# Kernel optimization log

Hardware: AMD Instinct MI355X
Metric: run time of the kernel (lower is better)

## Reference

```python
import jax, jax.numpy as jnp
import numpy as np

N_JOINT = 32
N_EDGE = N_JOINT * (N_JOINT - 1)  # 992, fully-connected directed, no self loops
IN_ENC = 150   # 3 * source_seq_len
NH, NO = 256, 128   # node hidden / node out (node_hidden_dim = edge_hidden_dim in source)
EH, EO = 256, 128   # edge hidden / edge out
DEC_IN = 3
T, B = 25, 16
NUM_PASSING = 2


def _incidence():
    send, rec = np.nonzero(~np.eye(N_JOINT, dtype=bool))
    R = np.zeros((N_EDGE, N_JOINT), np.float32)
    S = np.zeros((N_EDGE, N_JOINT), np.float32)
    R[np.arange(N_EDGE), rec] = 1.0
    S[np.arange(N_EDGE), send] = 1.0
    return jnp.asarray(R), jnp.asarray(S)


def _mlp(x, w1, b1, w2, b2):
    # Linear -> ReLU -> (Dropout p=0) -> Linear -> ReLU
    return jax.nn.relu(jax.nn.relu(x @ w1 + b1) @ w2 + b2)


def _node2edge(x, R, S):
    # x: [B, N, D] -> [B, E, 2D] (sends then recs, as in source)
    sends = jnp.einsum('en,bnd->bed', S, x)
    recs = jnp.einsum('en,bnd->bed', R, x)
    return jnp.concatenate([sends, recs], axis=-1)


def _edge2node(x, R):
    # x: [B, E, D] -> [B, N, D], mean over incoming edges
    inc = jnp.einsum('en,bed->bnd', R, x)
    return inc / R.sum(0)[:, None]


def setup_inputs() -> dict:
    key = jax.random.key(0)
    ks = jax.random.split(key, 24)
    R, S = _incidence()

    def lin(k, i, o):
        return jax.random.normal(k, (i, o), jnp.float32) * (2.0 / (i + o)) ** 0.5

    b = lambda o: jnp.full((o,), 0.1, jnp.float32)
    inp = {
        'encoder_input': jax.random.normal(ks[0], (B, N_JOINT, IN_ENC), jnp.float32),
        'decoder_input': jax.random.normal(ks[1], (T, B, N_JOINT, DEC_IN), jnp.float32),
        'rec_encode': R, 'send_encode': S,
        # encoder mlp1: IN_ENC -> NH -> NO
        'enc_w1': lin(ks[2], IN_ENC, NH), 'enc_b1': b(NH),
        'enc_w2': lin(ks[3], NH, NO), 'enc_b2': b(NO),
        # passing edge MLP: 2*NO -> EH -> EO
        'pe_w1': lin(ks[4], 2 * NO, EH), 'pe_b1': b(EH),
        'pe_w2': lin(ks[5], EH, EO), 'pe_b2': b(EO),
        # passing node MLP: EO -> NH -> NO
        'pn_w1': lin(ks[6], EO, NH), 'pn_b1': b(NH),
        'pn_w2': lin(ks[7], NH, NO), 'pn_b2': b(NO),
        # decoder node2edge MLP: 2*NO -> EH -> EO
        'de_w1': lin(ks[8], 2 * NO, EH), 'de_b1': b(EH),
        'de_w2': lin(ks[9], EH, EO), 'de_b2': b(EO),
        # GRU-like gates; input_size = DEC_IN + EO
        'w_hr': lin(ks[10], NO, NO), 'w_hi': lin(ks[11], NO, NO), 'w_hn': lin(ks[12], NO, NO),
        'w_ir': lin(ks[13], EO + DEC_IN, NO), 'b_ir': b(NO),
        'w_ii': lin(ks[14], EO + DEC_IN, NO), 'b_ii': b(NO),
        'w_in': lin(ks[15], EO + DEC_IN, NO), 'b_in': b(NO),
    }
    return inp


def reference(encoder_input, decoder_input, rec_encode, send_encode,
              enc_w1, enc_b1, enc_w2, enc_b2,
              pe_w1, pe_b1, pe_w2, pe_b2,
              pn_w1, pn_b1, pn_w2, pn_b2,
              de_w1, de_b1, de_w2, de_b2,
              w_hr, w_hi, w_hn, w_ir, b_ir, w_ii, b_ii, w_in, b_in):
    R, S = rec_encode, send_encode
    # ---- encoder ----
    x = _mlp(encoder_input, enc_w1, enc_b1, enc_w2, enc_b2)  # [B,N,NO]
    for _ in range(NUM_PASSING):
        x = _mlp(_node2edge(x, R, S), pe_w1, pe_b1, pe_w2, pe_b2)  # [B,E,EO]
        x = _mlp(_edge2node(x, R), pn_w1, pn_b1, pn_w2, pn_b2)     # [B,N,NO]
    node_hidden = x

    # ---- decoder: GRU-style recurrent message passing ----
    def step(h, inp):
        e = _mlp(_node2edge(h, R, S), de_w1, de_b1, de_w2, de_b2)  # [B,E,EO]
        msg = _edge2node(e, R)                                      # [B,N,EO]
        ni = jnp.concatenate([msg, inp], axis=-1)                   # [B,N,EO+3]
        r = jax.nn.sigmoid(ni @ w_ir + b_ir + h @ w_hr)
        i = jax.nn.sigmoid(ni @ w_ii + b_ii + h @ w_hi)
        n = jnp.tanh(ni @ w_in + b_in + r * (h @ w_hn))
        h_new = (1.0 - i) * n + i * h
        return h_new, h_new

    state, outputs = jax.lax.scan(step, node_hidden, decoder_input)
    return outputs, state
```

## Files before the change

kernel.cpp:

```cpp
#include <hip/hip_runtime.h>


#define TSTEPS 25

typedef _Float16 half_t;
typedef __attribute__((ext_vector_type(8))) _Float16 half8;
typedef __attribute__((ext_vector_type(8))) short short8;
typedef __attribute__((ext_vector_type(4))) float f32x4;

#define OFF_ENC_W1T 0
#define OFF_ENC_W2T 40960
#define OFF_PE_W1T  73728
#define OFF_PE_W2T  139264
#define OFF_PN_W1T  172032
#define OFF_PN_W2T  204800
#define OFF_DE_W1T  237568
#define OFF_DE_W2T  303104
#define OFF_WGT     335872
#define WTOTAL      483328

__device__ __align__(16) half_t g_wf16[WTOTAL];
__device__ __align__(16) float g_hbuf[2 * 512 * 128];
__device__ __align__(16) float g_msg[512 * 128];

__device__ __forceinline__ half8 h8zero() {
    half8 z;
    #pragma unroll
    for (int e = 0; e < 8; ++e) z[e] = (half_t)0.f;
    return z;
}
__device__ __forceinline__ half8 relu8(half8 x) {
    short8 s = *(short8*)&x;
    short8 m = s >> 15;
    s = s & ~m;
    return *(half8*)&s;
}
#define MFMA(a, b, c) __builtin_amdgcn_mfma_f32_16x16x32_f16((a), (b), (c), 0, 0, 0)
#define BFRAG(off, tile, KS, kk) ((off) + (((tile) * (KS) + (kk)) << 9) + m16 * 32 + quad * 8)

__global__ void convert_kernel(const float* __restrict__ enc_w1, const float* __restrict__ enc_w2,
                               const float* __restrict__ pe_w1, const float* __restrict__ pe_w2,
                               const float* __restrict__ pn_w1, const float* __restrict__ pn_w2,
                               const float* __restrict__ de_w1, const float* __restrict__ de_w2,
                               const float* __restrict__ w_hr, const float* __restrict__ w_hi,
                               const float* __restrict__ w_hn, const float* __restrict__ w_ir,
                               const float* __restrict__ w_ii, const float* __restrict__ w_in) {
    const int idx = blockIdx.x * 256 + threadIdx.x;
    if (idx >= WTOTAL) return;
    float v = 0.f;
    if (idx < OFF_ENC_W2T) {
        int s = idx, e = s & 7, quad = (s >> 3) & 3, m16 = (s >> 5) & 15, t = s >> 9;
        int kk = t % 5, nt = t / 5;
        int j = nt * 16 + m16, k = kk * 32 + quad * 8 + e;
        v = (k < 150) ? enc_w1[k * 256 + j] : 0.f;
    } else if (idx < OFF_PE_W1T) {
        int s = idx - OFF_ENC_W2T, e = s & 7, quad = (s >> 3) & 3, m16 = (s >> 5) & 15, t = s >> 9;
        int kk = t & 7, nt = t >> 3;
        int j = nt * 16 + m16, k = kk * 32 + quad * 8 + e;
        v = enc_w2[k * 128 + j];
    } else if (idx < OFF_PE_W2T) {
        int s = idx - OFF_PE_W1T, e = s & 7, quad = (s >> 3) & 3, m16 = (s >> 5) & 15, t = s >> 9;
        int kk = t & 3, nt = t >> 2;
        int j = nt * 16 + m16, k = kk * 32 + quad * 8 + e;
        v = pe_w1[(k + ((j >= 256) ? 128 : 0)) * 256 + (j & 255)];
    } else if (idx < OFF_PN_W1T) {
        int s = idx - OFF_PE_W2T, e = s & 7, quad = (s >> 3) & 3, m16 = (s >> 5) & 15, t = s >> 9;
        int kk = t & 7, nt = t >> 3;
        int j = nt * 16 + m16, k = kk * 32 + quad * 8 + e;
        v = pe_w2[k * 128 + j];
    } else if (idx < OFF_PN_W2T) {
        int s = idx - OFF_PN_W1T, e = s & 7, quad = (s >> 3) & 3, m16 = (s >> 5) & 15, t = s >> 9;
        int kk = t & 3, nt = t >> 2;
        int j = nt * 16 + m16, k = kk * 32 + quad * 8 + e;
        v = pn_w1[k * 256 + j];
    } else if (idx < OFF_DE_W1T) {
        int s = idx - OFF_PN_W2T, e = s & 7, quad = (s >> 3) & 3, m16 = (s >> 5) & 15, t = s >> 9;
        int kk = t & 7, nt = t >> 3;
        int j = nt * 16 + m16, k = kk * 32 + quad * 8 + e;
        v = pn_w2[k * 128 + j];
    } else if (idx < OFF_DE_W2T) {
        int s = idx - OFF_DE_W1T, e = s & 7, quad = (s >> 3) & 3, m16 = (s >> 5) & 15, t = s >> 9;
        int kk = t & 3, nt = t >> 2;
        int j = nt * 16 + m16, k = kk * 32 + quad * 8 + e;
        v = de_w1[(k + ((j >= 256) ? 128 : 0)) * 256 + (j & 255)];
    } else if (idx < OFF_WGT) {
        int s = idx - OFF_DE_W1T - (OFF_DE_W2T - OFF_DE_W1T), e = s & 7, quad = (s >> 3) & 3, m16 = (s >> 5) & 15, t = s >> 9;
        int kk = t & 7, nt = t >> 3;
        int j = nt * 16 + m16, k = kk * 32 + quad * 8 + e;
        v = de_w2[k * 128 + j];
    } else {
        int s = idx - OFF_WGT, e = s & 7, quad = (s >> 3) & 3, m16 = (s >> 5) & 15, t = s >> 9;
        int kk = t % 9, ct = t / 9;
        int c = ct * 16 + m16, k = kk * 32 + quad * 8 + e;
        int grp = (c >> 5) & 3, j = ((c >> 7) << 5) | (c & 31);
        if (grp == 0)
            v = (k < 128) ? w_ir[k * 128 + j] : (k < 256) ? w_hr[(k - 128) * 128 + j]
              : (k < 259) ? w_ir[(128 + k - 256) * 128 + j] : 0.f;
        else if (grp == 1)
            v = (k < 128) ? w_ii[k * 128 + j] : (k < 256) ? w_hi[(k - 128) * 128 + j]
              : (k < 259) ? w_ii[(128 + k - 256) * 128 + j] : 0.f;
        else if (grp == 2)
            v = (k < 128) ? w_in[k * 128 + j]
              : (k >= 256 && k < 259) ? w_in[(128 + k - 256) * 128 + j] : 0.f;
        else
            v = (k >= 128 && k < 256) ? w_hn[(k - 128) * 128 + j] : 0.f;
    }
    g_wf16[idx] = (half_t)v;
}

__global__ void __launch_bounds__(512, 2)
encoder_kernel(const float* __restrict__ enc_in,
               const float* __restrict__ enc_b1, const float* __restrict__ enc_b2) {
    const int b = blockIdx.x & 15;
    const int sub = blockIdx.x >> 4;
    const int tid = threadIdx.x;
    const int wave = tid >> 6;
    const int lane = tid & 63;
    const int m16 = lane & 15, quad = lane >> 4;
    const int r0 = sub * 4;

    __shared__ __align__(16) half_t s_enc[32 * 168];
    __shared__ __align__(16) half_t s_hid[32 * 264];

    for (int i = tid; i < 32 * 168; i += 512) {
        const int s = i / 168, k = i - s * 168;
        s_enc[i] = (half_t)((k < 150) ? enc_in[((size_t)b * 32 + s) * 150 + k] : 0.f);
    }
    __syncthreads();
    #pragma unroll
    for (int i = 0; i < 4; ++i) {
        const int ti = wave + i * 8;
        const int nt = ti & 15, mt = ti >> 4;
        f32x4 acc = (f32x4)(0.f);
        #pragma unroll
        for (int k = 0; k < 5; ++k) {
            half8 a  = *(const half8*)&s_enc[(mt * 16 + m16) * 168 + k * 32 + quad * 8];
            half8 bf = *(const half8*)&g_wf16[BFRAG(OFF_ENC_W1T, nt, 5, k)];
            acc = MFMA(a, bf, acc);
        }
        const int j = nt * 16 + m16;
        const float bj = enc_b1[j];
        #pragma unroll
        for (int g = 0; g < 4; ++g)
            s_hid[(mt * 16 + quad * 4 + g) * 264 + j] = (half_t)fmaxf(acc[g] + bj, 0.f);
    }
    __syncthreads();
    float* h0 = g_hbuf + (size_t)b * 32 * 128;
    #pragma unroll
    for (int i = 0; i < 2; ++i) {
        const int ti = wave + i * 8;
        const int nt = ti & 7, mt = ti >> 3;
        f32x4 acc = (f32x4)(0.f);
        #pragma unroll
        for (int k = 0; k < 8; ++k) {
            half8 a  = *(const half8*)&s_hid[(mt * 16 + m16) * 264 + k * 32 + quad * 8];
            half8 bf = *(const half8*)&g_wf16[BFRAG(OFF_ENC_W2T, nt, 8, k)];
            acc = MFMA(a, bf, acc);
        }
        if (mt == (sub >> 2) && quad == (sub & 3)) {
            const int j = nt * 16 + m16;
            const float bj = enc_b2[j];
            #pragma unroll
            for (int g = 0; g < 4; ++g)
                h0[(r0 + g) * 128 + j] = fmaxf(acc[g] + bj, 0.f);
        }
    }
}

template <int IS_DEC>
__global__ void __launch_bounds__(512, 1)
edge_kernel(int parity, const float* __restrict__ b1, const float* __restrict__ b2) {
    const int b = blockIdx.x >> 4;
    const int rq = blockIdx.x & 15;
    const int r0 = rq * 2;
    const int tid = threadIdx.x;
    const int wave = tid >> 6;
    const int lane = tid & 63;
    const int m16 = lane & 15, quad = lane >> 4;

    __shared__ __align__(16) half_t s_hh[32 * 136];
    __shared__ __align__(16) half_t s_P[32 * 264];
    __shared__ __align__(16) half_t s_Qb[2 * 264];

    {
        const float* hsrc = g_hbuf + (size_t)parity * 512 * 128 + (size_t)b * 32 * 128;
        const int i = tid * 8;
        const int row = i >> 7, col = i & 127;
        const float* sp = hsrc + row * 128 + col;
        half8 h0;
        #pragma unroll
        for (int e = 0; e < 8; ++e) h0[e] = (half_t)sp[e];
        *(half8*)&s_hh[row * 136 + col] = h0;
    }
    __syncthreads();

    {
        const int woff = IS_DEC ? OFF_DE_W1T : OFF_PE_W1T;
        const int rmt = r0 >> 4, rloc0 = r0 & 15;
        #pragma unroll
        for (int i = 0; i < 6; ++i) {
            const int ti = wave + 8 * i;
            const bool isQ = ti >= 32;
            const int nt = isQ ? (ti - 32) : (ti & 15);
            const int mt = isQ ? rmt : (ti >> 4);
            const int brow = isQ ? (nt + 16) : nt;
            f32x4 acc = (f32x4)(0.f);
            #pragma unroll
            for (int k = 0; k < 4; ++k) {
                half8 a = *(const half8*)&s_hh[(mt * 16 + m16) * 136 + k * 32 + quad * 8];
                half8 bf = *(const half8*)&g_wf16[BFRAG(woff, brow, 4, k)];
                acc = MFMA(a, bf, acc);
            }
            const int j = nt * 16 + m16;
            if (!isQ) {
                #pragma unroll
                for (int g = 0; g < 4; ++g)
                    s_P[(mt * 16 + quad * 4 + g) * 264 + j] = (half_t)acc[g];
            } else {
                const float bj = b1[j];
                #pragma unroll
                for (int g = 0; g < 4; ++g) {
                    const int rr = quad * 4 + g;
                    if (rr == rloc0)     s_Qb[j] = (half_t)(acc[g] + bj);
                    if (rr == rloc0 + 1) s_Qb[264 + j] = (half_t)(acc[g] + bj);
                }
            }
        }
    }
    __syncthreads();

    {
        const int woff2 = IS_DEC ? OFF_DE_W2T : OFF_PE_W2T;
        const int nt = wave;
        half8 qb[2][8];
        #pragma unroll
        for (int ri = 0; ri < 2; ++ri)
            #pragma unroll
            for (int k = 0; k < 8; ++k)
                qb[ri][k] = *(const half8*)&s_Qb[ri * 264 + k * 32 + quad * 8];
        f32x4 acc[2][2];
        #pragma unroll
        for (int ri = 0; ri < 2; ++ri)
            #pragma unroll
            for (int mt = 0; mt < 2; ++mt) acc[ri][mt] = (f32x4)(0.f);
        #pragma unroll
        for (int k = 0; k < 8; ++k) {
            half8 bf = *(const half8*)&g_wf16[BFRAG(woff2, nt, 8, k)];
            #pragma unroll
            for (int mt = 0; mt < 2; ++mt) {
                half8 pv = *(const half8*)&s_P[(mt * 16 + m16) * 264 + k * 32 + quad * 8];
                #pragma unroll
                for (int ri = 0; ri < 2; ++ri) {
                    half8 hv = relu8(pv + qb[ri][k]);
                    if (mt * 16 + m16 == r0 + ri) hv = h8zero();
                    acc[ri][mt] = MFMA(hv, bf, acc[ri][mt]);
                }
            }
        }
        const float b2n = b2[nt * 16 + m16];
        #pragma unroll
        for (int ri = 0; ri < 2; ++ri) {
            float pp = 0.f;
            #pragma unroll
            for (int mt = 0; mt < 2; ++mt)
                #pragma unroll
                for (int g = 0; g < 4; ++g)
                    pp += fmaxf(acc[ri][mt][g] + b2n, 0.f);
            pp += __shfl_xor(pp, 16);
            pp += __shfl_xor(pp, 32);
            if (quad == 0)
                g_msg[((size_t)b * 32 + r0 + ri) * 128 + nt * 16 + m16] =
                    (pp - fmaxf(b2n, 0.f)) * (1.f / 31.f);
        }
    }
}

__global__ void __launch_bounds__(256, 4)
node_kernel(int parity_out, const float* __restrict__ pn_b1, const float* __restrict__ pn_b2) {
    const int mt16 = blockIdx.x;
    const int tid = threadIdx.x;
    const int wave = tid >> 6;
    const int lane = tid & 63;
    const int m16 = lane & 15, quad = lane >> 4;

    __shared__ __align__(16) half_t s_A[16 * 136];
    __shared__ __align__(16) half_t s_H[16 * 264];

    {
        const int i = tid * 8;
        const int row = i >> 7, col = i & 127;
        const float* sp = g_msg + ((size_t)mt16 * 16 + row) * 128 + col;
        half8 h0;
        #pragma unroll
        for (int e = 0; e < 8; ++e) h0[e] = (half_t)sp[e];
        *(half8*)&s_A[row * 136 + col] = h0;
    }
    __syncthreads();
    #pragma unroll
    for (int i = 0; i < 4; ++i) {
        const int nt = wave + 4 * i;
        f32x4 acc = (f32x4)(0.f);
        #pragma unroll
        for (int k = 0; k < 4; ++k) {
            half8 a = *(const half8*)&s_A[m16 * 136 + k * 32 + quad * 8];
            half8 bf = *(const half8*)&g_wf16[BFRAG(OFF_PN_W1T, nt, 4, k)];
            acc = MFMA(a, bf, acc);
        }
        const int j = nt * 16 + m16;
        const float bj = pn_b1[j];
        #pragma unroll
        for (int g = 0; g < 4; ++g)
            s_H[(quad * 4 + g) * 264 + j] = (half_t)fmaxf(acc[g] + bj, 0.f);
    }
    __syncthreads();
    float* h_next = g_hbuf + (size_t)parity_out * 512 * 128;
    #pragma unroll
    for (int i = 0; i < 2; ++i) {
        const int nt = wave + 4 * i;
        f32x4 acc = (f32x4)(0.f);
        #pragma unroll
        for (int k = 0; k < 8; ++k) {
            half8 a = *(const half8*)&s_H[m16 * 264 + k * 32 + quad * 8];
            half8 bf = *(const half8*)&g_wf16[BFRAG(OFF_PN_W2T, nt, 8, k)];
            acc = MFMA(a, bf, acc);
        }
        const int j = nt * 16 + m16;
        const float bj = pn_b2[j];
        #pragma unroll
        for (int g = 0; g < 4; ++g)
            h_next[((size_t)mt16 * 16 + quad * 4 + g) * 128 + j] = fmaxf(acc[g] + bj, 0.f);
    }
}

__global__ void __launch_bounds__(256, 4)
gru_kernel(int parity, int t,
           const float* __restrict__ b_ir, const float* __restrict__ b_ii,
           const float* __restrict__ b_in,
           const float* __restrict__ dec_in, float* __restrict__ out) {
    const int b = blockIdx.x >> 3;
    const int nt = (blockIdx.x >> 1) & 3;
    const int mt2 = blockIdx.x & 1;
    const int rbase = mt2 * 16;
    const int tid = threadIdx.x;
    const int wave = tid >> 6;
    const int lane = tid & 63;
    const int m16 = lane & 15, quad = lane >> 4;
    const float* hsrc = g_hbuf + (size_t)parity * 512 * 128 + (size_t)b * 32 * 128;

    __shared__ __align__(16) half_t s_A[16 * 296];
    __shared__ __align__(16) half_t s_g[16 * 136];

    {
        const int i = tid * 8;
        const int row = i >> 7, col = i & 127;
        const float* mp = g_msg + ((size_t)b * 32 + rbase + row) * 128 + col;
        const float* hp = hsrc + (rbase + row) * 128 + col;
        half8 m0, h0;
        #pragma unroll
        for (int e = 0; e < 8; ++e) { m0[e] = (half_t)mp[e]; h0[e] = (half_t)hp[e]; }
        *(half8*)&s_A[row * 296 + col] = m0;
        *(half8*)&s_A[row * 296 + 128 + col] = h0;
    }
    for (int i = tid; i < 16 * 32; i += 256) {
        const int row = i >> 5, c = i & 31;
        s_A[row * 296 + 256 + c] = (c < 3)
            ? (half_t)dec_in[(((size_t)t * 16 + b) * 32 + rbase + row) * 3 + c] : (half_t)0.f;
    }
    __syncthreads();

    #pragma unroll
    for (int i = 0; i < 2; ++i) {
        const int nt2 = wave + 4 * i;
        const int ct = nt * 8 + nt2;
        f32x4 acc = (f32x4)(0.f);
        #pragma unroll
        for (int k = 0; k < 9; ++k) {
            half8 a = *(const half8*)&s_A[m16 * 296 + k * 32 + quad * 8];
            half8 bf = *(const half8*)&g_wf16[BFRAG(OFF_WGT, ct, 9, k)];
            acc = MFMA(a, bf, acc);
        }
        #pragma unroll
        for (int g = 0; g < 4; ++g)
            s_g[(quad * 4 + g) * 136 + nt2 * 16 + m16] = (half_t)acc[g];
    }
    __syncthreads();

    float* h_next = g_hbuf + (size_t)(parity ^ 1) * 512 * 128 + (size_t)b * 32 * 128;
    #pragma unroll
    for (int e = 0; e < 2; ++e) {
        const int idx = tid + 256 * e;
        const int row = idx >> 5, jl = idx & 31;
        const int j = nt * 32 + jl;
        const float rs = (float)s_g[row * 136 + jl] + b_ir[j];
        const float is = (float)s_g[row * 136 + 32 + jl] + b_ii[j];
        const float ns = (float)s_g[row * 136 + 64 + jl] + b_in[j];
        const float hn = (float)s_g[row * 136 + 96 + jl];
        const float rr = 1.f / (1.f + __expf(-rs));
        const float ii = 1.f / (1.f + __expf(-is));
        const float nn = tanhf(ns + rr * hn);
        const float hold = hsrc[(rbase + row) * 128 + j];
        const float hnew = (1.f - ii) * nn + ii * hold;
        h_next[(rbase + row) * 128 + j] = hnew;
        const size_t grow = (size_t)b * 32 + rbase + row;
        out[(size_t)t * 512 * 128 + grow * 128 + j] = hnew;
        if (t == TSTEPS - 1)
            out[(size_t)TSTEPS * 512 * 128 + grow * 128 + j] = hnew;
    }
}

extern "C" void kernel_launch(void* const* d_in, const int* in_sizes, int n_in,
                              void* d_out, int out_size, void* d_ws, size_t ws_size,
                              hipStream_t stream) {
    const float* enc_in = (const float*)d_in[0];
    const float* dec_in = (const float*)d_in[1];
    const float* enc_w1 = (const float*)d_in[4];
    const float* enc_b1 = (const float*)d_in[5];
    const float* enc_w2 = (const float*)d_in[6];
    const float* enc_b2 = (const float*)d_in[7];
    const float* pe_w1 = (const float*)d_in[8];
    const float* pe_b1 = (const float*)d_in[9];
    const float* pe_w2 = (const float*)d_in[10];
    const float* pe_b2 = (const float*)d_in[11];
    const float* pn_w1 = (const float*)d_in[12];
    const float* pn_b1 = (const float*)d_in[13];
    const float* pn_w2 = (const float*)d_in[14];
    const float* pn_b2 = (const float*)d_in[15];
    const float* de_w1 = (const float*)d_in[16];
    const float* de_b1 = (const float*)d_in[17];
    const float* de_w2 = (const float*)d_in[18];
    const float* de_b2 = (const float*)d_in[19];
    const float* w_hr = (const float*)d_in[20];
    const float* w_hi = (const float*)d_in[21];
    const float* w_hn = (const float*)d_in[22];
    const float* w_ir = (const float*)d_in[23];
    const float* b_ir = (const float*)d_in[24];
    const float* w_ii = (const float*)d_in[25];
    const float* b_ii = (const float*)d_in[26];
    const float* w_in = (const float*)d_in[27];
    const float* b_in = (const float*)d_in[28];
    (void)d_ws; (void)ws_size; (void)in_sizes; (void)n_in;

    convert_kernel<<<(WTOTAL + 255) / 256, 256, 0, stream>>>(
        enc_w1, enc_w2, pe_w1, pe_w2, pn_w1, pn_w2, de_w1, de_w2,
        w_hr, w_hi, w_hn, w_ir, w_ii, w_in);

    encoder_kernel<<<128, 512, 0, stream>>>(enc_in, enc_b1, enc_b2);

    int p = 0;
    for (int pass = 0; pass < 2; ++pass) {
        edge_kernel<0><<<256, 512, 0, stream>>>(p, pe_b1, pe_b2);
        node_kernel<<<32, 256, 0, stream>>>(p ^ 1, pn_b1, pn_b2);
        p ^= 1;
    }
    float* out = (float*)d_out;
    for (int t = 0; t < TSTEPS; ++t) {
        edge_kernel<1><<<256, 512, 0, stream>>>(p, de_b1, de_b2);
        gru_kernel<<<128, 256, 0, stream>>>(p, t, b_ir, b_ii, b_in, dec_in, out);
        p ^= 1;
    }
}
```

Baseline: 445.4 us.

## Fuse node MLP and GRU update into edge kernel, dropping global message buffer

Folds the node MLP (encoder passes) and the GRU gate computation (decoder steps) into the edge kernel's epilogue. Each block keeps its two-row message in shared memory and runs the follow-up MFMAs on padded 16-row tiles where only 2 rows are valid. This halves the number of kernel launches per step and removes the g_msg round trip through global memory. In exchange, much of the follow-up MFMA work is spent on zero rows, and every block re-reads the gate and node weights.

```diff
diff --git a/kernel.cpp b/kernel.cpp
--- a/kernel.cpp
+++ b/kernel.cpp
@@ -21,7 +21,6 @@
 
 __device__ __align__(16) half_t g_wf16[WTOTAL];
 __device__ __align__(16) float g_hbuf[2 * 512 * 128];
-__device__ __align__(16) float g_msg[512 * 128];
 
 __device__ __forceinline__ half8 h8zero() {
     half8 z;
@@ -34,6 +33,14 @@
     short8 m = s >> 15;
     s = s & ~m;
     return *(half8*)&s;
+}
+__device__ __forceinline__ half8 frag_from_f32(const float* base) {
+    f32x4 a = *(const f32x4*)base;
+    f32x4 c = *(const f32x4*)(base + 4);
+    half8 h;
+    #pragma unroll
+    for (int e = 0; e < 4; ++e) { h[e] = (half_t)a[e]; h[4 + e] = (half_t)c[e]; }
+    return h;
 }
 #define MFMA(a, b, c) __builtin_amdgcn_mfma_f32_16x16x32_f16((a), (b), (c), 0, 0, 0)
 #define BFRAG(off, tile, KS, kk) ((off) + (((tile) * (KS) + (kk)) << 9) + m16 * 32 + quad * 8)
@@ -84,7 +91,7 @@
         int j = nt * 16 + m16, k = kk * 32 + quad * 8 + e;
         v = de_w1[(k + ((j >= 256) ? 128 : 0)) * 256 + (j & 255)];
     } else if (idx < OFF_WGT) {
-        int s = idx - OFF_DE_W1T - (OFF_DE_W2T - OFF_DE_W1T), e = s & 7, quad = (s >> 3) & 3, m16 = (s >> 5) & 15, t = s >> 9;
+        int s = idx - OFF_DE_W2T, e = s & 7, quad = (s >> 3) & 3, m16 = (s >> 5) & 15, t = s >> 9;
         int kk = t & 7, nt = t >> 3;
         int j = nt * 16 + m16, k = kk * 32 + quad * 8 + e;
         v = de_w2[k * 128 + j];
@@ -169,7 +176,11 @@
 
 template <int IS_DEC>
 __global__ void __launch_bounds__(512, 1)
-edge_kernel(int parity, const float* __restrict__ b1, const float* __restrict__ b2) {
+step_kernel(int parity, int t,
+            const float* __restrict__ b1, const float* __restrict__ b2,
+            const float* __restrict__ nb1_or_ir, const float* __restrict__ nb2_or_ii,
+            const float* __restrict__ b_in,
+            const float* __restrict__ dec_in, float* __restrict__ out) {
     const int b = blockIdx.x >> 4;
     const int rq = blockIdx.x & 15;
     const int r0 = rq * 2;
@@ -181,9 +192,15 @@
     __shared__ __align__(16) half_t s_hh[32 * 136];
     __shared__ __align__(16) half_t s_P[32 * 264];
     __shared__ __align__(16) half_t s_Qb[2 * 264];
+    __shared__ __align__(16) float  s_msg[2 * 128];
+    __shared__ __align__(16) half_t s_aux[2 * 304];
+    __shared__ __align__(16) half_t s_hid[2 * 264];
+    __shared__ __align__(16) float  s_g[2 * 512];
+
+    const float* hsrc = g_hbuf + (size_t)parity * 512 * 128 + (size_t)b * 32 * 128;
+    float* h_next = g_hbuf + (size_t)(parity ^ 1) * 512 * 128 + (size_t)b * 32 * 128;
 
     {
-        const float* hsrc = g_hbuf + (size_t)parity * 512 * 128 + (size_t)b * 32 * 128;
         const int i = tid * 8;
         const int row = i >> 7, col = i & 127;
         const float* sp = hsrc + row * 128 + col;
@@ -269,142 +286,100 @@
             pp += __shfl_xor(pp, 16);
             pp += __shfl_xor(pp, 32);
             if (quad == 0)
-                g_msg[((size_t)b * 32 + r0 + ri) * 128 + nt * 16 + m16] =
-                    (pp - fmaxf(b2n, 0.f)) * (1.f / 31.f);
-        }
-    }
-}
-
-__global__ void __launch_bounds__(256, 4)
-node_kernel(int parity_out, const float* __restrict__ pn_b1, const float* __restrict__ pn_b2) {
-    const int mt16 = blockIdx.x;
-    const int tid = threadIdx.x;
-    const int wave = tid >> 6;
-    const int lane = tid & 63;
-    const int m16 = lane & 15, quad = lane >> 4;
-
-    __shared__ __align__(16) half_t s_A[16 * 136];
-    __shared__ __align__(16) half_t s_H[16 * 264];
-
-    {
-        const int i = tid * 8;
-        const int row = i >> 7, col = i & 127;
-        const float* sp = g_msg + ((size_t)mt16 * 16 + row) * 128 + col;
-        half8 h0;
-        #pragma unroll
-        for (int e = 0; e < 8; ++e) h0[e] = (half_t)sp[e];
-        *(half8*)&s_A[row * 136 + col] = h0;
+                s_msg[ri * 128 + nt * 16 + m16] = (pp - fmaxf(b2n, 0.f)) * (1.f / 31.f);
+        }
     }
     __syncthreads();
-    #pragma unroll
-    for (int i = 0; i < 4; ++i) {
-        const int nt = wave + 4 * i;
-        f32x4 acc = (f32x4)(0.f);
-        #pragma unroll
-        for (int k = 0; k < 4; ++k) {
-            half8 a = *(const half8*)&s_A[m16 * 136 + k * 32 + quad * 8];
-            half8 bf = *(const half8*)&g_wf16[BFRAG(OFF_PN_W1T, nt, 4, k)];
-            acc = MFMA(a, bf, acc);
-        }
-        const int j = nt * 16 + m16;
-        const float bj = pn_b1[j];
-        #pragma unroll
-        for (int g = 0; g < 4; ++g)
-            s_H[(quad * 4 + g) * 264 + j] = (half_t)fmaxf(acc[g] + bj, 0.f);
-    }
-    __syncthreads();
-    float* h_next = g_hbuf + (size_t)parity_out * 512 * 128;
-    #pragma unroll
-    for (int i = 0; i < 2; ++i) {
-        const int nt = wave + 4 * i;
-        f32x4 acc = (f32x4)(0.f);
-        #pragma unroll
-        for (int k = 0; k < 8; ++k) {
-            half8 a = *(const half8*)&s_H[m16 * 264 + k * 32 + quad * 8];
-            half8 bf = *(const half8*)&g_wf16[BFRAG(OFF_PN_W2T, nt, 8, k)];
-            acc = MFMA(a, bf, acc);
-        }
-        const int j = nt * 16 + m16;
-        const float bj = pn_b2[j];
-        #pragma unroll
-        for (int g = 0; g < 4; ++g)
-            h_next[((size_t)mt16 * 16 + quad * 4 + g) * 128 + j] = fmaxf(acc[g] + bj, 0.f);
-    }
-}
-
-__global__ void __launch_bounds__(256, 4)
-gru_kernel(int parity, int t,
-           const float* __restrict__ b_ir, const float* __restrict__ b_ii,
-           const float* __restrict__ b_in,
-           const float* __restrict__ dec_in, float* __restrict__ out) {
-    const int b = blockIdx.x >> 3;
-    const int nt = (blockIdx.x >> 1) & 3;
-    const int mt2 = blockIdx.x & 1;
-    const int rbase = mt2 * 16;
-    const int tid = threadIdx.x;
-    const int wave = tid >> 6;
-    const int lane = tid & 63;
-    const int m16 = lane & 15, quad = lane >> 4;
-    const float* hsrc = g_hbuf + (size_t)parity * 512 * 128 + (size_t)b * 32 * 128;
-
-    __shared__ __align__(16) half_t s_A[16 * 296];
-    __shared__ __align__(16) half_t s_g[16 * 136];
-
-    {
-        const int i = tid * 8;
-        const int row = i >> 7, col = i & 127;
-        const float* mp = g_msg + ((size_t)b * 32 + rbase + row) * 128 + col;
-        const float* hp = hsrc + (rbase + row) * 128 + col;
-        half8 m0, h0;
-        #pragma unroll
-        for (int e = 0; e < 8; ++e) { m0[e] = (half_t)mp[e]; h0[e] = (half_t)hp[e]; }
-        *(half8*)&s_A[row * 296 + col] = m0;
-        *(half8*)&s_A[row * 296 + 128 + col] = h0;
-    }
-    for (int i = tid; i < 16 * 32; i += 256) {
-        const int row = i >> 5, c = i & 31;
-        s_A[row * 296 + 256 + c] = (c < 3)
-            ? (half_t)dec_in[(((size_t)t * 16 + b) * 32 + rbase + row) * 3 + c] : (half_t)0.f;
-    }
-    __syncthreads();
-
-    #pragma unroll
-    for (int i = 0; i < 2; ++i) {
-        const int nt2 = wave + 4 * i;
-        const int ct = nt * 8 + nt2;
-        f32x4 acc = (f32x4)(0.f);
-        #pragma unroll
-        for (int k = 0; k < 9; ++k) {
-            half8 a = *(const half8*)&s_A[m16 * 296 + k * 32 + quad * 8];
-            half8 bf = *(const half8*)&g_wf16[BFRAG(OFF_WGT, ct, 9, k)];
-            acc = MFMA(a, bf, acc);
-        }
-        #pragma unroll
-        for (int g = 0; g < 4; ++g)
-            s_g[(quad * 4 + g) * 136 + nt2 * 16 + m16] = (half_t)acc[g];
-    }
-    __syncthreads();
-
-    float* h_next = g_hbuf + (size_t)(parity ^ 1) * 512 * 128 + (size_t)b * 32 * 128;
-    #pragma unroll
-    for (int e = 0; e < 2; ++e) {
-        const int idx = tid + 256 * e;
-        const int row = idx >> 5, jl = idx & 31;
-        const int j = nt * 32 + jl;
-        const float rs = (float)s_g[row * 136 + jl] + b_ir[j];
-        const float is = (float)s_g[row * 136 + 32 + jl] + b_ii[j];
-        const float ns = (float)s_g[row * 136 + 64 + jl] + b_in[j];
-        const float hn = (float)s_g[row * 136 + 96 + jl];
-        const float rr = 1.f / (1.f + __expf(-rs));
-        const float ii = 1.f / (1.f + __expf(-is));
-        const float nn = tanhf(ns + rr * hn);
-        const float hold = hsrc[(rbase + row) * 128 + j];
-        const float hnew = (1.f - ii) * nn + ii * hold;
-        h_next[(rbase + row) * 128 + j] = hnew;
-        const size_t grow = (size_t)b * 32 + rbase + row;
-        out[(size_t)t * 512 * 128 + grow * 128 + j] = hnew;
-        if (t == TSTEPS - 1)
-            out[(size_t)TSTEPS * 512 * 128 + grow * 128 + j] = hnew;
+
+    if (!IS_DEC) {
+        half8 a1[4];
+        #pragma unroll
+        for (int k = 0; k < 4; ++k)
+            a1[k] = (m16 < 2) ? frag_from_f32(&s_msg[m16 * 128 + k * 32 + quad * 8])
+                              : h8zero();
+        #pragma unroll
+        for (int i = 0; i < 2; ++i) {
+            const int nt = wave + 8 * i;
+            f32x4 acc = (f32x4)(0.f);
+            #pragma unroll
+            for (int k = 0; k < 4; ++k)
+                acc = MFMA(a1[k], *(const half8*)&g_wf16[BFRAG(OFF_PN_W1T, nt, 4, k)], acc);
+            if (quad == 0) {
+                const int j = nt * 16 + m16;
+                const float bj = nb1_or_ir[j];
+                #pragma unroll
+                for (int g = 0; g < 2; ++g)
+                    s_hid[g * 264 + j] = (half_t)fmaxf(acc[g] + bj, 0.f);
+            }
+        }
+        __syncthreads();
+        half8 a2[8];
+        #pragma unroll
+        for (int k = 0; k < 8; ++k)
+            a2[k] = (m16 < 2) ? *(const half8*)&s_hid[m16 * 264 + k * 32 + quad * 8]
+                              : h8zero();
+        {
+            const int nt = wave;
+            f32x4 acc = (f32x4)(0.f);
+            #pragma unroll
+            for (int k = 0; k < 8; ++k)
+                acc = MFMA(a2[k], *(const half8*)&g_wf16[BFRAG(OFF_PN_W2T, nt, 8, k)], acc);
+            if (quad == 0) {
+                const int j = nt * 16 + m16;
+                const float bj = nb2_or_ii[j];
+                #pragma unroll
+                for (int g = 0; g < 2; ++g)
+                    h_next[(r0 + g) * 128 + j] = fmaxf(acc[g] + bj, 0.f);
+            }
+        }
+    } else {
+        for (int i = tid; i < 2 * 304; i += 512) {
+            const int row = i / 304, c = i - row * 304;
+            half_t v = (half_t)0.f;
+            if (c < 128) v = (half_t)s_msg[row * 128 + c];
+            else if (c < 256) v = s_hh[(r0 + row) * 136 + (c - 128)];
+            else if (c < 259)
+                v = (half_t)dec_in[(((size_t)t * 16 + b) * 32 + r0 + row) * 3 + (c - 256)];
+            s_aux[row * 304 + c] = v;
+        }
+        __syncthreads();
+        half8 ag[9];
+        #pragma unroll
+        for (int k = 0; k < 9; ++k)
+            ag[k] = (m16 < 2) ? *(const half8*)&s_aux[m16 * 304 + k * 32 + quad * 8]
+                              : h8zero();
+        #pragma unroll
+        for (int i = 0; i < 4; ++i) {
+            const int ct = wave + 8 * i;
+            f32x4 acc = (f32x4)(0.f);
+            #pragma unroll
+            for (int k = 0; k < 9; ++k)
+                acc = MFMA(ag[k], *(const half8*)&g_wf16[BFRAG(OFF_WGT, ct, 9, k)], acc);
+            if (quad == 0) {
+                #pragma unroll
+                for (int g = 0; g < 2; ++g)
+                    s_g[g * 512 + ct * 16 + m16] = acc[g];
+            }
+        }
+        __syncthreads();
+        if (tid < 256) {
+            const int row = tid >> 7, j = tid & 127;
+            const int cb = ((j >> 5) << 7) | (j & 31);
+            const float rs = s_g[row * 512 + cb + 0] + nb1_or_ir[j];
+            const float is = s_g[row * 512 + cb + 32] + nb2_or_ii[j];
+            const float ns = s_g[row * 512 + cb + 64] + b_in[j];
+            const float hn = s_g[row * 512 + cb + 96];
+            const float rr = 1.f / (1.f + __expf(-rs));
+            const float ii = 1.f / (1.f + __expf(-is));
+            const float nn = tanhf(ns + rr * hn);
+            const float hold = hsrc[(r0 + row) * 128 + j];
+            const float hnew = (1.f - ii) * nn + ii * hold;
+            h_next[(r0 + row) * 128 + j] = hnew;
+            const size_t grow = (size_t)b * 32 + r0 + row;
+            out[(size_t)t * 512 * 128 + grow * 128 + j] = hnew;
+            if (t == TSTEPS - 1)
+                out[(size_t)TSTEPS * 512 * 128 + grow * 128 + j] = hnew;
+        }
     }
 }
 
@@ -448,14 +423,14 @@
 
     int p = 0;
     for (int pass = 0; pass < 2; ++pass) {
-        edge_kernel<0><<<256, 512, 0, stream>>>(p, pe_b1, pe_b2);
-        node_kernel<<<32, 256, 0, stream>>>(p ^ 1, pn_b1, pn_b2);
+        step_kernel<0><<<256, 512, 0, stream>>>(p, 0, pe_b1, pe_b2, pn_b1, pn_b2,
+                                                nullptr, nullptr, nullptr);
         p ^= 1;
     }
     float* out = (float*)d_out;
     for (int t = 0; t < TSTEPS; ++t) {
-        edge_kernel<1><<<256, 512, 0, stream>>>(p, de_b1, de_b2);
-        gru_kernel<<<128, 256, 0, stream>>>(p, t, b_ir, b_ii, b_in, dec_in, out);
+        step_kernel<1><<<256, 512, 0, stream>>>(p, t, de_b1, de_b2, b_ir, b_ii,
+                                                b_in, dec_in, out);
         p ^= 1;
     }
 }
```

After: 451.8 us. No clear change (+1.5%).

## Move edge first-layer P/Q projection into producer kernels via global fp16 buffers

Applied to the files above, without the earlier changes.

The per-node first-layer projections (P for all rows, Q plus bias) that each of the 16 edge blocks per batch recomputed are now computed once in the encoder, node and GRU kernels and written to global fp16 buffers. Edge kernels only load them, which removes redundant MFMA work across 256 blocks. The GRU and node kernels are restructured so each block covers 16 full rows with 512 threads, keeping the whole row available for the fused projection. The ping-pong h buffer becomes a single buffer. This adds global traffic for P/Q and reduces GRU grid parallelism from 128 to 32 blocks.

```diff
diff --git a/kernel.cpp b/kernel.cpp
--- a/kernel.cpp
+++ b/kernel.cpp
@@ -20,8 +20,10 @@
 #define WTOTAL      483328
 
 __device__ __align__(16) half_t g_wf16[WTOTAL];
-__device__ __align__(16) float g_hbuf[2 * 512 * 128];
-__device__ __align__(16) float g_msg[512 * 128];
+__device__ __align__(16) float  g_h[512 * 128];
+__device__ __align__(16) half_t g_P[512 * 256];
+__device__ __align__(16) half_t g_Qb[512 * 256];
+__device__ __align__(16) float  g_msg[512 * 128];
 
 __device__ __forceinline__ half8 h8zero() {
     half8 z;
@@ -84,7 +86,7 @@
         int j = nt * 16 + m16, k = kk * 32 + quad * 8 + e;
         v = de_w1[(k + ((j >= 256) ? 128 : 0)) * 256 + (j & 255)];
     } else if (idx < OFF_WGT) {
-        int s = idx - OFF_DE_W1T - (OFF_DE_W2T - OFF_DE_W1T), e = s & 7, quad = (s >> 3) & 3, m16 = (s >> 5) & 15, t = s >> 9;
+        int s = idx - OFF_DE_W2T, e = s & 7, quad = (s >> 3) & 3, m16 = (s >> 5) & 15, t = s >> 9;
         int kk = t & 7, nt = t >> 3;
         int j = nt * 16 + m16, k = kk * 32 + quad * 8 + e;
         v = de_w2[k * 128 + j];
@@ -108,124 +110,118 @@
     g_wf16[idx] = (half_t)v;
 }
 
+template <int NW>
+__device__ __forceinline__ void pq_tail(const half_t* s_hh, int w1off,
+                                        const float* __restrict__ b1,
+                                        int growbase, int wave, int m16, int quad) {
+    half8 a[4];
+    #pragma unroll
+    for (int k = 0; k < 4; ++k)
+        a[k] = *(const half8*)&s_hh[m16 * 136 + k * 32 + quad * 8];
+    #pragma unroll
+    for (int i = 0; i < 32 / NW; ++i) {
+        const int nt = wave + NW * i;
+        f32x4 acc = (f32x4)(0.f);
+        #pragma unroll
+        for (int k = 0; k < 4; ++k)
+            acc = MFMA(a[k], *(const half8*)&g_wf16[BFRAG(w1off, nt, 4, k)], acc);
+        if (nt < 16) {
+            const int j = nt * 16 + m16;
+            #pragma unroll
+            for (int g = 0; g < 4; ++g)
+                g_P[(size_t)(growbase + quad * 4 + g) * 256 + j] = (half_t)acc[g];
+        } else {
+            const int j = (nt - 16) * 16 + m16;
+            const float bj = b1[j];
+            #pragma unroll
+            for (int g = 0; g < 4; ++g)
+                g_Qb[(size_t)(growbase + quad * 4 + g) * 256 + j] = (half_t)(acc[g] + bj);
+        }
+    }
+}
+
 __global__ void __launch_bounds__(512, 2)
 encoder_kernel(const float* __restrict__ enc_in,
-               const float* __restrict__ enc_b1, const float* __restrict__ enc_b2) {
-    const int b = blockIdx.x & 15;
-    const int sub = blockIdx.x >> 4;
+               const float* __restrict__ enc_b1, const float* __restrict__ enc_b2,
+               const float* __restrict__ pe_b1) {
+    const int b = blockIdx.x >> 1;
+    const int rbase = (blockIdx.x & 1) * 16;
+    const int growbase = b * 32 + rbase;
     const int tid = threadIdx.x;
     const int wave = tid >> 6;
     const int lane = tid & 63;
     const int m16 = lane & 15, quad = lane >> 4;
-    const int r0 = sub * 4;
-
-    __shared__ __align__(16) half_t s_enc[32 * 168];
-    __shared__ __align__(16) half_t s_hid[32 * 264];
-
-    for (int i = tid; i < 32 * 168; i += 512) {
+
+    __shared__ __align__(16) half_t s_enc[16 * 168];
+    __shared__ __align__(16) half_t s_hid[16 * 264];
+    __shared__ __align__(16) half_t s_hh[16 * 136];
+
+    for (int i = tid; i < 16 * 168; i += 512) {
         const int s = i / 168, k = i - s * 168;
-        s_enc[i] = (half_t)((k < 150) ? enc_in[((size_t)b * 32 + s) * 150 + k] : 0.f);
-    }
-    __syncthreads();
-    #pragma unroll
-    for (int i = 0; i < 4; ++i) {
-        const int ti = wave + i * 8;
-        const int nt = ti & 15, mt = ti >> 4;
+        s_enc[i] = (half_t)((k < 150) ? enc_in[(size_t)(growbase + s) * 150 + k] : 0.f);
+    }
+    __syncthreads();
+    #pragma unroll
+    for (int i = 0; i < 2; ++i) {
+        const int nt = wave + 8 * i;
         f32x4 acc = (f32x4)(0.f);
         #pragma unroll
         for (int k = 0; k < 5; ++k) {
-            half8 a  = *(const half8*)&s_enc[(mt * 16 + m16) * 168 + k * 32 + quad * 8];
-            half8 bf = *(const half8*)&g_wf16[BFRAG(OFF_ENC_W1T, nt, 5, k)];
-            acc = MFMA(a, bf, acc);
+            half8 a = *(const half8*)&s_enc[m16 * 168 + k * 32 + quad * 8];
+            acc = MFMA(a, *(const half8*)&g_wf16[BFRAG(OFF_ENC_W1T, nt, 5, k)], acc);
         }
         const int j = nt * 16 + m16;
         const float bj = enc_b1[j];
         #pragma unroll
         for (int g = 0; g < 4; ++g)
-            s_hid[(mt * 16 + quad * 4 + g) * 264 + j] = (half_t)fmaxf(acc[g] + bj, 0.f);
-    }
-    __syncthreads();
-    float* h0 = g_hbuf + (size_t)b * 32 * 128;
-    #pragma unroll
-    for (int i = 0; i < 2; ++i) {
-        const int ti = wave + i * 8;
-        const int nt = ti & 7, mt = ti >> 3;
+            s_hid[(quad * 4 + g) * 264 + j] = (half_t)fmaxf(acc[g] + bj, 0.f);
+    }
+    __syncthreads();
+    {
+        const int nt = wave;
         f32x4 acc = (f32x4)(0.f);
         #pragma unroll
         for (int k = 0; k < 8; ++k) {
-            half8 a  = *(const half8*)&s_hid[(mt * 16 + m16) * 264 + k * 32 + quad * 8];
-            half8 bf = *(const half8*)&g_wf16[BFRAG(OFF_ENC_W2T, nt, 8, k)];
-            acc = MFMA(a, bf, acc);
-        }
-        if (mt == (sub >> 2) && quad == (sub & 3)) {
-            const int j = nt * 16 + m16;
-            const float bj = enc_b2[j];
-            #pragma unroll
-            for (int g = 0; g < 4; ++g)
-                h0[(r0 + g) * 128 + j] = fmaxf(acc[g] + bj, 0.f);
-        }
-    }
+            half8 a = *(const half8*)&s_hid[m16 * 264 + k * 32 + quad * 8];
+            acc = MFMA(a, *(const half8*)&g_wf16[BFRAG(OFF_ENC_W2T, nt, 8, k)], acc);
+        }
+        const int j = nt * 16 + m16;
+        const float bj = enc_b2[j];
+        #pragma unroll
+        for (int g = 0; g < 4; ++g) {
+            const float hv = fmaxf(acc[g] + bj, 0.f);
+            g_h[(size_t)(growbase + quad * 4 + g) * 128 + j] = hv;
+            s_hh[(quad * 4 + g) * 136 + j] = (half_t)hv;
+        }
+    }
+    __syncthreads();
+    pq_tail<8>(s_hh, OFF_PE_W1T, pe_b1, growbase, wave, m16, quad);
 }
 
 template <int IS_DEC>
-__global__ void __launch_bounds__(512, 1)
-edge_kernel(int parity, const float* __restrict__ b1, const float* __restrict__ b2) {
+__global__ void __launch_bounds__(512, 2)
+edge_kernel(const float* __restrict__ b2) {
     const int b = blockIdx.x >> 4;
-    const int rq = blockIdx.x & 15;
-    const int r0 = rq * 2;
+    const int r0 = (blockIdx.x & 15) * 2;
     const int tid = threadIdx.x;
     const int wave = tid >> 6;
     const int lane = tid & 63;
     const int m16 = lane & 15, quad = lane >> 4;
 
-    __shared__ __align__(16) half_t s_hh[32 * 136];
     __shared__ __align__(16) half_t s_P[32 * 264];
     __shared__ __align__(16) half_t s_Qb[2 * 264];
 
     {
-        const float* hsrc = g_hbuf + (size_t)parity * 512 * 128 + (size_t)b * 32 * 128;
-        const int i = tid * 8;
-        const int row = i >> 7, col = i & 127;
-        const float* sp = hsrc + row * 128 + col;
-        half8 h0;
-        #pragma unroll
-        for (int e = 0; e < 8; ++e) h0[e] = (half_t)sp[e];
-        *(half8*)&s_hh[row * 136 + col] = h0;
-    }
-    __syncthreads();
-
-    {
-        const int woff = IS_DEC ? OFF_DE_W1T : OFF_PE_W1T;
-        const int rmt = r0 >> 4, rloc0 = r0 & 15;
-        #pragma unroll
-        for (int i = 0; i < 6; ++i) {
-            const int ti = wave + 8 * i;
-            const bool isQ = ti >= 32;
-            const int nt = isQ ? (ti - 32) : (ti & 15);
-            const int mt = isQ ? rmt : (ti >> 4);
-            const int brow = isQ ? (nt + 16) : nt;
-            f32x4 acc = (f32x4)(0.f);
-            #pragma unroll
-            for (int k = 0; k < 4; ++k) {
-                half8 a = *(const half8*)&s_hh[(mt * 16 + m16) * 136 + k * 32 + quad * 8];
-                half8 bf = *(const half8*)&g_wf16[BFRAG(woff, brow, 4, k)];
-                acc = MFMA(a, bf, acc);
-            }
-            const int j = nt * 16 + m16;
-            if (!isQ) {
-                #pragma unroll
-                for (int g = 0; g < 4; ++g)
-                    s_P[(mt * 16 + quad * 4 + g) * 264 + j] = (half_t)acc[g];
-            } else {
-                const float bj = b1[j];
-                #pragma unroll
-                for (int g = 0; g < 4; ++g) {
-                    const int rr = quad * 4 + g;
-                    if (rr == rloc0)     s_Qb[j] = (half_t)(acc[g] + bj);
-                    if (rr == rloc0 + 1) s_Qb[264 + j] = (half_t)(acc[g] + bj);
-                }
-            }
-        }
+        const int i = tid * 16;
+        const int row = i >> 8, col = i & 255;
+        const half_t* sp = g_P + (size_t)(b * 32 + row) * 256 + col;
+        *(half8*)&s_P[row * 264 + col] = *(const half8*)sp;
+        *(half8*)&s_P[row * 264 + col + 8] = *(const half8*)(sp + 8);
+    }
+    if (tid < 64) {
+        const int ri = tid >> 5, col = (tid & 31) * 8;
+        *(half8*)&s_Qb[ri * 264 + col] =
+            *(const half8*)&g_Qb[(size_t)(b * 32 + r0 + ri) * 256 + col];
     }
     __syncthreads();
 
@@ -269,27 +265,30 @@
             pp += __shfl_xor(pp, 16);
             pp += __shfl_xor(pp, 32);
             if (quad == 0)
-                g_msg[((size_t)b * 32 + r0 + ri) * 128 + nt * 16 + m16] =
+                g_msg[(size_t)(b * 32 + r0 + ri) * 128 + nt * 16 + m16] =
                     (pp - fmaxf(b2n, 0.f)) * (1.f / 31.f);
         }
     }
 }
 
-__global__ void __launch_bounds__(256, 4)
-node_kernel(int parity_out, const float* __restrict__ pn_b1, const float* __restrict__ pn_b2) {
-    const int mt16 = blockIdx.x;
+template <int NEXT_DE>
+__global__ void __launch_bounds__(512, 2)
+node_kernel(const float* __restrict__ pn_b1, const float* __restrict__ pn_b2,
+            const float* __restrict__ next_b1) {
+    const int growbase = blockIdx.x * 16;
     const int tid = threadIdx.x;
     const int wave = tid >> 6;
     const int lane = tid & 63;
     const int m16 = lane & 15, quad = lane >> 4;
 
     __shared__ __align__(16) half_t s_A[16 * 136];
-    __shared__ __align__(16) half_t s_H[16 * 264];
-
-    {
+    __shared__ __align__(16) half_t s_hid[16 * 264];
+    __shared__ __align__(16) half_t s_hh[16 * 136];
+
+    if (tid < 256) {
         const int i = tid * 8;
         const int row = i >> 7, col = i & 127;
-        const float* sp = g_msg + ((size_t)mt16 * 16 + row) * 128 + col;
+        const float* sp = g_msg + (size_t)(growbase + row) * 128 + col;
         half8 h0;
         #pragma unroll
         for (int e = 0; e < 8; ++e) h0[e] = (half_t)sp[e];
@@ -297,114 +296,117 @@
     }
     __syncthreads();
     #pragma unroll
-    for (int i = 0; i < 4; ++i) {
-        const int nt = wave + 4 * i;
+    for (int i = 0; i < 2; ++i) {
+        const int nt = wave + 8 * i;
         f32x4 acc = (f32x4)(0.f);
         #pragma unroll
         for (int k = 0; k < 4; ++k) {
             half8 a = *(const half8*)&s_A[m16 * 136 + k * 32 + quad * 8];
-            half8 bf = *(const half8*)&g_wf16[BFRAG(OFF_PN_W1T, nt, 4, k)];
-            acc = MFMA(a, bf, acc);
+            acc = MFMA(a, *(const half8*)&g_wf16[BFRAG(OFF_PN_W1T, nt, 4, k)], acc);
         }
         const int j = nt * 16 + m16;
         const float bj = pn_b1[j];
         #pragma unroll
         for (int g = 0; g < 4; ++g)
-            s_H[(quad * 4 + g) * 264 + j] = (half_t)fmaxf(acc[g] + bj, 0.f);
-    }
-    __syncthreads();
-    float* h_next = g_hbuf + (size_t)parity_out * 512 * 128;
-    #pragma unroll
-    for (int i = 0; i < 2; ++i) {
-        const int nt = wave + 4 * i;
+            s_hid[(quad * 4 + g) * 264 + j] = (half_t)fmaxf(acc[g] + bj, 0.f);
+    }
+    __syncthreads();
+    {
+        const int nt = wave;
         f32x4 acc = (f32x4)(0.f);
         #pragma unroll
         for (int k = 0; k < 8; ++k) {
-            half8 a = *(const half8*)&s_H[m16 * 264 + k * 32 + quad * 8];
-            half8 bf = *(const half8*)&g_wf16[BFRAG(OFF_PN_W2T, nt, 8, k)];
-            acc = MFMA(a, bf, acc);
+            half8 a = *(const half8*)&s_hid[m16 * 264 + k * 32 + quad * 8];
+            acc = MFMA(a, *(const half8*)&g_wf16[BFRAG(OFF_PN_W2T, nt, 8, k)], acc);
         }
         const int j = nt * 16 + m16;
         const float bj = pn_b2[j];
         #pragma unroll
-        for (int g = 0; g < 4; ++g)
-            h_next[((size_t)mt16 * 16 + quad * 4 + g) * 128 + j] = fmaxf(acc[g] + bj, 0.f);
-    }
-}
-
-__global__ void __launch_bounds__(256, 4)
-gru_kernel(int parity, int t,
+        for (int g = 0; g < 4; ++g) {
+            const float hv = fmaxf(acc[g] + bj, 0.f);
+            g_h[(size_t)(growbase + quad * 4 + g) * 128 + j] = hv;
+            s_hh[(quad * 4 + g) * 136 + j] = (half_t)hv;
+        }
+    }
+    __syncthreads();
+    pq_tail<8>(s_hh, NEXT_DE ? OFF_DE_W1T : OFF_PE_W1T, next_b1, growbase,
+               wave, m16, quad);
+}
+
+__global__ void __launch_bounds__(512, 2)
+gru_kernel(int t,
            const float* __restrict__ b_ir, const float* __restrict__ b_ii,
-           const float* __restrict__ b_in,
+           const float* __restrict__ b_in, const float* __restrict__ de_b1,
            const float* __restrict__ dec_in, float* __restrict__ out) {
-    const int b = blockIdx.x >> 3;
-    const int nt = (blockIdx.x >> 1) & 3;
-    const int mt2 = blockIdx.x & 1;
-    const int rbase = mt2 * 16;
+    const int b = blockIdx.x >> 1;
+    const int rbase = (blockIdx.x & 1) * 16;
+    const int growbase = b * 32 + rbase;
     const int tid = threadIdx.x;
     const int wave = tid >> 6;
     const int lane = tid & 63;
     const int m16 = lane & 15, quad = lane >> 4;
-    const float* hsrc = g_hbuf + (size_t)parity * 512 * 128 + (size_t)b * 32 * 128;
 
     __shared__ __align__(16) half_t s_A[16 * 296];
-    __shared__ __align__(16) half_t s_g[16 * 136];
+    __shared__ __align__(16) float  s_g[16 * 520];
+    __shared__ __align__(16) half_t s_hh[16 * 136];
 
     {
-        const int i = tid * 8;
+        const int i = (tid & 255) * 8;
         const int row = i >> 7, col = i & 127;
-        const float* mp = g_msg + ((size_t)b * 32 + rbase + row) * 128 + col;
-        const float* hp = hsrc + (rbase + row) * 128 + col;
-        half8 m0, h0;
-        #pragma unroll
-        for (int e = 0; e < 8; ++e) { m0[e] = (half_t)mp[e]; h0[e] = (half_t)hp[e]; }
-        *(half8*)&s_A[row * 296 + col] = m0;
-        *(half8*)&s_A[row * 296 + 128 + col] = h0;
-    }
-    for (int i = tid; i < 16 * 32; i += 256) {
-        const int row = i >> 5, c = i & 31;
+        const float* sp = (tid < 256)
+            ? g_msg + (size_t)(growbase + row) * 128 + col
+            : g_h + (size_t)(growbase + row) * 128 + col;
+        half8 h0;
+        #pragma unroll
+        for (int e = 0; e < 8; ++e) h0[e] = (half_t)sp[e];
+        *(half8*)&s_A[row * 296 + ((tid < 256) ? col : 128 + col)] = h0;
+    }
+    for (int i = tid; i < 16 * 40; i += 512) {
+        const int row = i / 40, c = i - row * 40;
         s_A[row * 296 + 256 + c] = (c < 3)
-            ? (half_t)dec_in[(((size_t)t * 16 + b) * 32 + rbase + row) * 3 + c] : (half_t)0.f;
-    }
-    __syncthreads();
-
-    #pragma unroll
-    for (int i = 0; i < 2; ++i) {
-        const int nt2 = wave + 4 * i;
-        const int ct = nt * 8 + nt2;
+            ? (half_t)dec_in[(size_t)((t * 16 + b) * 32 + rbase + row) * 3 + c]
+            : (half_t)0.f;
+    }
+    __syncthreads();
+
+    #pragma unroll
+    for (int i = 0; i < 4; ++i) {
+        const int ct = wave + 8 * i;
         f32x4 acc = (f32x4)(0.f);
         #pragma unroll
         for (int k = 0; k < 9; ++k) {
             half8 a = *(const half8*)&s_A[m16 * 296 + k * 32 + quad * 8];
-            half8 bf = *(const half8*)&g_wf16[BFRAG(OFF_WGT, ct, 9, k)];
-            acc = MFMA(a, bf, acc);
+            acc = MFMA(a, *(const half8*)&g_wf16[BFRAG(OFF_WGT, ct, 9, k)], acc);
         }
         #pragma unroll
         for (int g = 0; g < 4; ++g)
-            s_g[(quad * 4 + g) * 136 + nt2 * 16 + m16] = (half_t)acc[g];
-    }
-    __syncthreads();
-
-    float* h_next = g_hbuf + (size_t)(parity ^ 1) * 512 * 128 + (size_t)b * 32 * 128;
-    #pragma unroll
-    for (int e = 0; e < 2; ++e) {
-        const int idx = tid + 256 * e;
-        const int row = idx >> 5, jl = idx & 31;
-        const int j = nt * 32 + jl;
-        const float rs = (float)s_g[row * 136 + jl] + b_ir[j];
-        const float is = (float)s_g[row * 136 + 32 + jl] + b_ii[j];
-        const float ns = (float)s_g[row * 136 + 64 + jl] + b_in[j];
-        const float hn = (float)s_g[row * 136 + 96 + jl];
+            s_g[(quad * 4 + g) * 520 + ct * 16 + m16] = acc[g];
+    }
+    __syncthreads();
+
+    #pragma unroll
+    for (int e = 0; e < 4; ++e) {
+        const int idx = tid + 512 * e;
+        const int row = idx >> 7, j = idx & 127;
+        const int cb = ((j >> 5) << 7) | (j & 31);
+        const float rs = s_g[row * 520 + cb + 0] + b_ir[j];
+        const float is = s_g[row * 520 + cb + 32] + b_ii[j];
+        const float ns = s_g[row * 520 + cb + 64] + b_in[j];
+        const float hn = s_g[row * 520 + cb + 96];
         const float rr = 1.f / (1.f + __expf(-rs));
         const float ii = 1.f / (1.f + __expf(-is));
         const float nn = tanhf(ns + rr * hn);
-        const float hold = hsrc[(rbase + row) * 128 + j];
+        const float hold = g_h[(size_t)(growbase + row) * 128 + j];
         const float hnew = (1.f - ii) * nn + ii * hold;
-        h_next[(rbase + row) * 128 + j] = hnew;
-        const size_t grow = (size_t)b * 32 + rbase + row;
-        out[(size_t)t * 512 * 128 + grow * 128 + j] = hnew;
+        g_h[(size_t)(growbase + row) * 128 + j] = hnew;
+        s_hh[row * 136 + j] = (half_t)hnew;
+        out[(size_t)t * 512 * 128 + (size_t)(growbase + row) * 128 + j] = hnew;
         if (t == TSTEPS - 1)
-            out[(size_t)TSTEPS * 512 * 128 + grow * 128 + j] = hnew;
+            out[(size_t)TSTEPS * 512 * 128 + (size_t)(growbase + row) * 128 + j] = hnew;
+    }
+    if (t < TSTEPS - 1) {
+        __syncthreads();
+        pq_tail<8>(s_hh, OFF_DE_W1T, de_b1, growbase, wave, m16, quad);
     }
 }
 
@@ -444,18 +446,16 @@
         enc_w1, enc_w2, pe_w1, pe_w2, pn_w1, pn_w2, de_w1, de_w2,
         w_hr, w_hi, w_hn, w_ir, w_ii, w_in);
 
-    encoder_kernel<<<128, 512, 0, stream>>>(enc_in, enc_b1, enc_b2);
-
-    int p = 0;
-    for (int pass = 0; pass < 2; ++pass) {
-        edge_kernel<0><<<256, 512, 0, stream>>>(p, pe_b1, pe_b2);
-        node_kernel<<<32, 256, 0, stream>>>(p ^ 1, pn_b1, pn_b2);
-        p ^= 1;
-    }
+    encoder_kernel<<<32, 512, 0, stream>>>(enc_in, enc_b1, enc_b2, pe_b1);
+
+    edge_kernel<0><<<256, 512, 0, stream>>>(pe_b2);
+    node_kernel<0><<<32, 512, 0, stream>>>(pn_b1, pn_b2, pe_b1);
+    edge_kernel<0><<<256, 512, 0, stream>>>(pe_b2);
+    node_kernel<1><<<32, 512, 0, stream>>>(pn_b1, pn_b2, de_b1);
+
     float* out = (float*)d_out;
     for (int t = 0; t < TSTEPS; ++t) {
-        edge_kernel<1><<<256, 512, 0, stream>>>(p, de_b1, de_b2);
-        gru_kernel<<<128, 256, 0, stream>>>(p, t, b_ir, b_ii, b_in, dec_in, out);
-        p ^= 1;
-    }
-}
+        edge_kernel<1><<<256, 512, 0, stream>>>(de_b2);
+        gru_kernel<<<32, 512, 0, stream>>>(t, b_ir, b_ii, b_in, de_b1, dec_in, out);
+    }
+}
```

Measured after the change: 504.1 us. +13.2%, slower.
